# Performance work log

Measured on AMD Instinct MI355X. Metric: run time of the kernel, lower is better.

Reference implementation:

```python
import jax, jax.numpy as jnp
import numpy as np
from jax.scipy.optimize import minimize

LAMDA = 0.01        # lamda default in MI()
N_DOMAINS = 2       # domain_label is binary (source/target)
MAXITER = 50        # BFGS iteration budget (torchmin l-bfgs analogue)


def _sq_dists(A, B):
    # squared euclidean pairwise distances == torch.cdist(A, B, p=2) ** 2
    an = jnp.sum(A * A, axis=-1)
    bn = jnp.sum(B * B, axis=-1)
    return an[:, None] + bn[None, :] - 2.0 * (A @ B.T)


def _median_sigma(sf):
    # sigma = median of nonzero squared pairwise source distances.
    # With continuous features the only zeros are the diagonal, so mask it.
    pd = jnp.maximum(_sq_dists(sf, sf), 0.0)
    pd = jnp.where(jnp.eye(pd.shape[0], dtype=bool), jnp.nan, pd)
    return jnp.nanmedian(pd)


def _build(sf, tf, y, l):
    # Gaussian kernel masked by class agreement, plus domain one-hots.
    sigma = _median_sigma(sf)
    X = jnp.concatenate([sf, tf], axis=0)              # [N, d]
    D = _sq_dists(X, X)                                 # [N, N]
    Deltay = (y[:, None] == y[None, :]).astype(X.dtype)
    K_W = jnp.exp(-D / sigma) * Deltay                  # [N, N]
    onehot = jax.nn.one_hot(l[:, 0], N_DOMAINS, dtype=X.dtype)  # [N, 2]
    KD = K_W * (onehot @ onehot.T)                      # K_W * Deltal
    w = jnp.sum(onehot, axis=0) / X.shape[0]            # domain counts / N
    return K_W, KD, onehot, w


def _div(theta, K_W, KD, onehot, w):
    # mean((K_W*Deltal) @ theta) - mean(exp((theta*K_W) @ Deltal - 1))
    # Deltal = onehot @ onehot.T (rank-2), so the second NxN @ NxN matmul
    # collapses to A = K_W @ (theta[:,None]*onehot) with column weights w.
    term1 = jnp.mean(KD @ theta)
    A = K_W @ (theta[:, None] * onehot)                 # [N, 2]
    term2 = jnp.mean(jnp.exp(A - 1.0) @ w)
    return term1 - term2


def _solve_theta(K_W, KD, onehot, w):
    N = K_W.shape[0]
    obj = lambda th: -_div(th, K_W, KD, onehot, w) + LAMDA * (th @ th)
    res = minimize(obj, jnp.zeros((N,), K_W.dtype), method="BFGS",
                   options={"maxiter": MAXITER})
    return res.x


def setup_inputs() -> dict:
    key = jax.random.key(0)
    k1, k2, k3, k4 = jax.random.split(key, 4)
    B, d, n_class = 2048, 256, 31
    source_features = jax.random.normal(k1, (B, d), dtype=jnp.float32)
    target_features = jax.random.normal(k2, (B, d), dtype=jnp.float32)
    y = jax.random.randint(k3, (2 * B,), 0, n_class, dtype=jnp.int32)
    l = jax.random.randint(k4, (2 * B, 1), 0, N_DOMAINS, dtype=jnp.int32)
    return {"source_features": source_features, "target_features": target_features,
            "y": y, "l": l}


def reference(source_features, target_features, y, l):
    K_W, KD, onehot, w = _build(source_features, target_features, y, l)
    theta_hat = _solve_theta(K_W, KD, onehot, w)
    return _div(theta_hat, K_W, KD, onehot, w)
```

## Files before the change

### kernel.cpp

```cpp
#include <hip/hip_runtime.h>
#include <math.h>

#define N_TOT   4096
#define N_SRC   2048
#define DIMF    256
#define NCLASS  31
#define LAMBDA  0.01f

#define K_TRI1  1048063LL
#define K_TRI2  1048064LL

#define WS_ACC    0
#define WS_HIST0  64
#define WS_HISTA  16448
#define WS_HISTB  32832
#define WS_H2A    49216
#define WS_H2B    50240
#define WS_STATE  51264
#define WS_TICK   51520
#define WS_META   52288
#define WS_SCAL   52800
#define ZERO_BYTES 53248
#define WS_PERM   53248
#define WS_XN     69632
#define WS_DS     1048576
#define WS_KBLK   17825792

#define MAXW 224
#define MAXM 112
#define WPAD 114

__device__ __forceinline__ float bf2f(unsigned short h) {
  return __uint_as_float(((unsigned)h) << 16);
}

__device__ __forceinline__ double blockReduceSum(double v, double* red) {
#pragma unroll
  for (int o = 32; o > 0; o >>= 1) v += __shfl_down(v, o, 64);
  int w = threadIdx.x >> 6, lane = threadIdx.x & 63;
  __syncthreads();
  if (lane == 0) red[w] = v;
  __syncthreads();
  return red[0] + red[1] + red[2] + red[3];
}

__device__ __forceinline__ void blockReduceSumMax(double s, double mx, double* red,
                                                  double& os, double& om) {
#pragma unroll
  for (int o = 32; o > 0; o >>= 1) {
    s += __shfl_down(s, o, 64);
    double u = __shfl_down(mx, o, 64);
    mx = fmax(mx, u);
  }
  int w = threadIdx.x >> 6, lane = threadIdx.x & 63;
  __syncthreads();
  if (lane == 0) { red[w] = s; red[4 + w] = mx; }
  __syncthreads();
  os = red[0] + red[1] + red[2] + red[3];
  om = fmax(fmax(red[4], red[5]), fmax(red[6], red[7]));
}

__device__ void scan_find(const unsigned* hist, int nbins, long long k, unsigned* shOut) {
  __shared__ long long tsum[256];
  int tid = threadIdx.x;
  int per = nbins / 256;
  long long s = 0;
  for (int q = 0; q < per; q++) s += hist[tid * per + q];
  tsum[tid] = s;
  __syncthreads();
  if (tid == 0) {
    long long run = 0;
    for (int t = 0; t < 256; t++) { long long v = tsum[t]; tsum[t] = run; run += v; }
  }
  __syncthreads();
  long long run = tsum[tid];
  for (int q = 0; q < per; q++) {
    unsigned c = hist[tid * per + q];
    if (k >= run && k < run + (long long)c) { shOut[0] = (unsigned)(tid * per + q); shOut[1] = (unsigned)(k - run); }
    run += c;
  }
  __syncthreads();
}

__global__ __launch_bounds__(256) void xn_kernel(const float* __restrict__ sf,
                                                 const float* __restrict__ tf,
                                                 float* __restrict__ xn) {
  int wid = threadIdx.x >> 6, lane = threadIdx.x & 63;
  int row = blockIdx.x * 4 + wid;
  const float* src = (row < N_SRC) ? (sf + (size_t)row * DIMF) : (tf + (size_t)(row - N_SRC) * DIMF);
  float4 v = ((const float4*)src)[lane];
  float s = v.x * v.x + v.y * v.y + v.z * v.z + v.w * v.w;
#pragma unroll
  for (int o = 32; o > 0; o >>= 1) s += __shfl_down(s, o, 64);
  if (lane == 0) xn[row] = s;
}

__global__ __launch_bounds__(256) void dist_k(const float* __restrict__ sf,
                                              const float* __restrict__ xn,
                                              float* __restrict__ Ds,
                                              unsigned* __restrict__ h) {
  __shared__ float As[16][68];
  __shared__ float Bs[16][68];
  __shared__ unsigned lh[4096];
  const int tx = threadIdx.x, ty = threadIdx.y;
  const int tid = ty * 16 + tx;
  for (int q = tid; q < 4096; q += 256) lh[q] = 0;
  int b = blockIdx.x;
  int by = (int)((sqrtf(8.f * (float)b + 1.f) - 1.f) * 0.5f);
  while ((by + 1) * (by + 2) / 2 <= b) ++by;
  while (by * (by + 1) / 2 > b) --by;
  int bx = b - by * (by + 1) / 2;
  const int R = by * 64, C = bx * 64;
  const int si = tid >> 2, sq = tid & 3;
  float4 va = ((const float4*)(sf + (size_t)(R + si) * 256 + 0))[sq];
  float4 vb = ((const float4*)(sf + (size_t)(C + si) * 256 + 0))[sq];
  float acc[4][4] = {};
  for (int kc = 0; kc < 256; kc += 16) {
    As[sq * 4 + 0][si] = va.x; As[sq * 4 + 1][si] = va.y; As[sq * 4 + 2][si] = va.z; As[sq * 4 + 3][si] = va.w;
    Bs[sq * 4 + 0][si] = vb.x; Bs[sq * 4 + 1][si] = vb.y; Bs[sq * 4 + 2][si] = vb.z; Bs[sq * 4 + 3][si] = vb.w;
    __syncthreads();
    if (kc + 16 < 256) {
      va = ((const float4*)(sf + (size_t)(R + si) * 256 + kc + 16))[sq];
      vb = ((const float4*)(sf + (size_t)(C + si) * 256 + kc + 16))[sq];
    }
#pragma unroll
    for (int k = 0; k < 16; k++) {
      float4 a = *(const float4*)&As[k][ty * 4];
      float4 b2 = *(const float4*)&Bs[k][tx * 4];
      acc[0][0] += a.x * b2.x; acc[0][1] += a.x * b2.y; acc[0][2] += a.x * b2.z; acc[0][3] += a.x * b2.w;
      acc[1][0] += a.y * b2.x; acc[1][1] += a.y * b2.y; acc[1][2] += a.y * b2.z; acc[1][3] += a.y * b2.w;
      acc[2][0] += a.z * b2.x; acc[2][1] += a.z * b2.y; acc[2][2] += a.z * b2.z; acc[2][3] += a.z * b2.w;
      acc[3][0] += a.w * b2.x; acc[3][1] += a.w * b2.y; acc[3][2] += a.w * b2.z; acc[3][3] += a.w * b2.w;
    }
    __syncthreads();
  }
  int jbase = C + tx * 4;
  float xnj0 = xn[jbase + 0], xnj1 = xn[jbase + 1], xnj2 = xn[jbase + 2], xnj3 = xn[jbase + 3];
#pragma unroll
  for (int r = 0; r < 4; r++) {
    int i = R + ty * 4 + r;
    float xni = xn[i];
    float v[4];
    v[0] = fmaxf(xni + xnj0 - 2.f * acc[r][0], 0.f);
    v[1] = fmaxf(xni + xnj1 - 2.f * acc[r][1], 0.f);
    v[2] = fmaxf(xni + xnj2 - 2.f * acc[r][2], 0.f);
    v[3] = fmaxf(xni + xnj3 - 2.f * acc[r][3], 0.f);
    if (jbase + 3 < i) {
      float4 o; o.x = v[0]; o.y = v[1]; o.z = v[2]; o.w = v[3];
      ((float4*)&Ds[(size_t)i * 2048 + jbase])[0] = o;
      atomicAdd(&lh[__float_as_uint(v[0]) >> 20], 1u);
      atomicAdd(&lh[__float_as_uint(v[1]) >> 20], 1u);
      atomicAdd(&lh[__float_as_uint(v[2]) >> 20], 1u);
      atomicAdd(&lh[__float_as_uint(v[3]) >> 20], 1u);
    } else {
#pragma unroll
      for (int k = 0; k < 4; k++) {
        if (jbase + k < i) {
          Ds[(size_t)i * 2048 + jbase + k] = v[k];
          atomicAdd(&lh[__float_as_uint(v[k]) >> 20], 1u);
        }
      }
    }
  }
  __syncthreads();
  for (int q = tid; q < 4096; q += 256) if (lh[q]) atomicAdd(&h[q], lh[q]);
}

__global__ __launch_bounds__(256) void scan0_k(const unsigned* __restrict__ h, unsigned* __restrict__ st) {
  __shared__ unsigned r0[2];
  __shared__ unsigned r1[2];
  scan_find(h, 4096, K_TRI1, r0);
  scan_find(h, 4096, K_TRI2, r1);
  if (threadIdx.x == 0) { st[0] = r0[0]; st[1] = r0[1]; st[2] = r1[0]; st[3] = r1[1]; }
}

__global__ __launch_bounds__(256) void hist1_k(const float* __restrict__ Ds, const unsigned* __restrict__ st,
                                               unsigned* __restrict__ hA, unsigned* __restrict__ hB) {
  __shared__ unsigned lA[4096];
  __shared__ unsigned lB[4096];
  for (int i = threadIdx.x; i < 4096; i += 256) { lA[i] = 0; lB[i] = 0; }
  __syncthreads();
  unsigned s0 = st[0], s1 = st[2];
  int gw = (blockIdx.x * 256 + threadIdx.x) >> 6;
  int lane = threadIdx.x & 63;
  const float* row = Ds + (size_t)gw * 2048;
  for (int j = lane; j < gw; j += 64) {
    unsigned u = __float_as_uint(row[j]);
    unsigned hi = u >> 20, mid = (u >> 8) & 0xFFFu;
    if (hi == s0) atomicAdd(&lA[mid], 1u);
    if (hi == s1) atomicAdd(&lB[mid], 1u);
  }
  __syncthreads();
  for (int i = threadIdx.x; i < 4096; i += 256) {
    if (lA[i]) atomicAdd(&hA[i], lA[i]);
    if (lB[i]) atomicAdd(&hB[i], lB[i]);
  }
}

__global__ __launch_bounds__(256) void scan1_k(const unsigned* __restrict__ hA, const unsigned* __restrict__ hB,
                                               unsigned* __restrict__ st) {
  __shared__ unsigned r0[2];
  __shared__ unsigned r1[2];
  long long kA = (long long)st[1];
  long long kB = (long long)st[3];
  scan_find(hA, 4096, kA, r0);
  scan_find(hB, 4096, kB, r1);
  if (threadIdx.x == 0) { st[4] = r0[0]; st[5] = r0[1]; st[6] = r1[0]; st[7] = r1[1]; }
}

__global__ __launch_bounds__(256) void hist2_k(const float* __restrict__ Ds, const unsigned* __restrict__ st,
                                               unsigned* __restrict__ hA, unsigned* __restrict__ hB) {
  __shared__ unsigned lA[256];
  __shared__ unsigned lB[256];
  lA[threadIdx.x] = 0; lB[threadIdx.x] = 0;
  __syncthreads();
  unsigned p0 = (st[0] << 12) | st[4];
  unsigned p1 = (st[2] << 12) | st[6];
  int gw = (blockIdx.x * 256 + threadIdx.x) >> 6;
  int lane = threadIdx.x & 63;
  const float* row = Ds + (size_t)gw * 2048;
  for (int j = lane; j < gw; j += 64) {
    unsigned u = __float_as_uint(row[j]);
    unsigned pre = u >> 8;
    if (pre == p0) atomicAdd(&lA[u & 0xFFu], 1u);
    if (pre == p1) atomicAdd(&lB[u & 0xFFu], 1u);
  }
  __syncthreads();
  if (lA[threadIdx.x]) atomicAdd(&hA[threadIdx.x], lA[threadIdx.x]);
  if (lB[threadIdx.x]) atomicAdd(&hB[threadIdx.x], lB[threadIdx.x]);
}

__global__ __launch_bounds__(256) void scan2b_k(const unsigned* __restrict__ hA, const unsigned* __restrict__ hB,
                                                const unsigned* __restrict__ st, float* __restrict__ scal,
                                                const int* __restrict__ y, const int* __restrict__ l,
                                                int* __restrict__ perm, int* __restrict__ meta) {
  int tid = threadIdx.x;
  __shared__ unsigned r0[2];
  __shared__ unsigned r1[2];
  scan_find(hA, 256, (long long)st[5], r0);
  scan_find(hB, 256, (long long)st[7], r1);
  if (tid == 0) {
    unsigned v1 = (st[0] << 20) | (st[4] << 8) | r0[0];
    unsigned v2 = (st[2] << 20) | (st[6] << 8) | r1[0];
    scal[0] = 0.5f * (__uint_as_float(v1) + __uint_as_float(v2));
  }
  __shared__ unsigned cl[64];
  __shared__ unsigned bs2[64];
  __shared__ unsigned cur[64];
  if (tid < 64) cl[tid] = 0;
  __syncthreads();
  for (int i = tid; i < N_TOT; i += 256) atomicAdd(&cl[y[i] * 2 + l[i]], 1u);
  __syncthreads();
  if (tid == 0) {
    unsigned run = 0;
    for (int b2 = 0; b2 < 62; b2++) { bs2[b2] = run; run += cl[b2]; }
    unsigned run2 = 0, cnt0 = 0;
    for (int c = 0; c < NCLASS; c++) {
      int n = (int)(cl[2 * c] + cl[2 * c + 1]);
      meta[c] = n; meta[32 + c] = (int)cl[2 * c]; meta[64 + c] = (int)bs2[2 * c];
      meta[96 + c] = (int)run2; run2 += (unsigned)(n * n);
      cnt0 += cl[2 * c];
    }
    scal[1] = (float)((double)cnt0 / (4096.0 * 4096.0));
    scal[2] = (float)((double)(N_TOT - cnt0) / (4096.0 * 4096.0));
  }
  __syncthreads();
  if (tid < 64) cur[tid] = bs2[tid];
  __syncthreads();
  for (int i = tid; i < N_TOT; i += 256) {
    int b2 = y[i] * 2 + l[i];
    unsigned pos = atomicAdd(&cur[b2], 1u);
    perm[pos] = i;
  }
}

__global__ __launch_bounds__(256) void build_k(const float* __restrict__ sf, const float* __restrict__ tf,
                                               const float* __restrict__ xn, const int* __restrict__ perm,
                                               const int* __restrict__ meta, const float* __restrict__ scal,
                                               float* __restrict__ gK) {
  const int c = blockIdx.z;
  const int n = meta[c];
  const int cs = meta[64 + c];
  const int bo = meta[96 + c];
  const int T = (n + 15) >> 4;
  int b = blockIdx.x;
  if (b >= T * (T + 1) / 2) return;
  int by = (int)((sqrtf(8.f * (float)b + 1.f) - 1.f) * 0.5f);
  while ((by + 1) * (by + 2) / 2 <= b) ++by;
  while (by * (by + 1) / 2 > b) --by;
  int bx = b - by * (by + 1) / 2;
  const int i0 = by * 16, j0 = bx * 16;
  const int tx = threadIdx.x, ty = threadIdx.y;
  __shared__ float As[16][260];
  __shared__ float Bs[16][260];
  __shared__ float ot[16][17];
  __shared__ int ra[16];
  __shared__ int rb[16];
  int tid = ty * 16 + tx;
  if (tid < 16) { int il = i0 + tid; ra[tid] = (il < n) ? perm[cs + il] : -1; }
  else if (tid < 32) { int jl = j0 + tid - 16; rb[tid - 16] = (jl < n) ? perm[cs + jl] : -1; }
  __syncthreads();
  for (int e = tid; e < 1024; e += 256) {
    int r = e >> 6, q = e & 63;
    int g = ra[r];
    if (g >= 0) {
      const float* src = (g < N_SRC) ? (sf + (size_t)g * DIMF) : (tf + (size_t)(g - N_SRC) * DIMF);
      ((float4*)&As[r][q * 4])[0] = ((const float4*)src)[q];
    }
    int g2 = rb[r];
    if (g2 >= 0) {
      const float* src = (g2 < N_SRC) ? (sf + (size_t)g2 * DIMF) : (tf + (size_t)(g2 - N_SRC) * DIMF);
      ((float4*)&Bs[r][q * 4])[0] = ((const float4*)src)[q];
    }
  }
  __syncthreads();
  int il = i0 + ty, jl = j0 + tx;
  float val = 0.f;
  if (il < n && jl < n) {
    float dot = 0.f;
    const float4* a4 = (const float4*)&As[ty][0];
    const float4* b4 = (const float4*)&Bs[tx][0];
#pragma unroll 16
    for (int q = 0; q < 64; q++) {
      float4 a = a4[q], b2 = b4[q];
      dot += a.x * b2.x + a.y * b2.y + a.z * b2.z + a.w * b2.w;
    }
    int gi = ra[ty], gj = rb[tx];
    float d = xn[gi] + xn[gj] - 2.f * dot;
    val = expf(-d / scal[0]);
    gK[(size_t)bo + (size_t)il * n + jl] = val;
  }
  ot[ty][tx] = val;
  __syncthreads();
  if (by != bx) {
    int il2 = j0 + ty, jl2 = i0 + tx;
    if (il2 < n && jl2 < n) gK[(size_t)bo + (size_t)il2 * n + jl2] = ot[tx][ty];
  }
}

__global__ __launch_bounds__(256) void solver_k(const float* __restrict__ gK, const int* __restrict__ meta,
                                                const float* __restrict__ scal, double* __restrict__ acc,
                                                unsigned* __restrict__ tick, float* __restrict__ out) {
  const int c = blockIdx.x >> 1, d = blockIdx.x & 1;
  const int n = meta[c];
  const int m0 = meta[32 + c];
  const int m = d ? (n - m0) : m0;
  const int c0 = d ? m0 : 0;
  const int bo = meta[96 + c];
  const float gamma = scal[1 + d];
  const int tid = threadIdx.x;
  const int wv = tid >> 6, lane = tid & 63;

  __shared__ unsigned short Wl[MAXW * WPAD];
  __shared__ float pS[4 * MAXM];
  __shared__ float pD[4 * MAXM];
  __shared__ float Av[MAXW];
  __shared__ float Sv[MAXW];
  __shared__ float Uv[MAXW];
  __shared__ float Bq[MAXW];
  __shared__ float bc[MAXM];
  __shared__ float th[MAXM + 1];
  __shared__ float gv[MAXM];
  __shared__ float dgv[MAXM];
  __shared__ float pv[MAXM + 1];
  __shared__ float rv[MAXM + 1];
  __shared__ float zv[MAXM + 1];
  __shared__ float xv[MAXM + 1];
  __shared__ double red[16];

  const float* K = gK + bo;
  const int st = n;
  const int mp2 = (m + 1) & ~1;
  const int iw0 = (n * wv) >> 2, iw1 = (n * (wv + 1)) >> 2;

  for (int i = tid >> 2; i < n; i += 64) {
    const float* Kr = K + (size_t)i * st + c0;
    unsigned short* Wr = Wl + i * WPAD;
    for (int j = (tid & 3); j < m; j += 4) {
      unsigned u = __float_as_uint(Kr[j]);
      u += 0x7fffu + ((u >> 16) & 1u);
      Wr[j] = (unsigned short)(u >> 16);
    }
    if ((tid & 3) == 0 && (m & 1)) Wr[m] = 0;
  }
  {
    const int r0 = (m * wv) >> 2, r1 = (m * (wv + 1)) >> 2;
    for (int j = lane; j < m; j += 64) {
      const float* Kr = K + (size_t)(c0 + j) * st + c0;
      float s = 0.f;
      for (int r = r0; r < r1; r++) s += Kr[r];
      pS[wv * MAXM + j] = s;
    }
  }
  __syncthreads();
  for (int j = tid; j < mp2; j += 256) {
    if (j < m) bc[j] = (pS[j] + pS[MAXM + j] + pS[2 * MAXM + j] + pS[3 * MAXM + j]) * (1.0f / 4096.0f);
    th[j] = 0.f;
  }
  __syncthreads();

  for (int it = 0; it < 25; it++) {
    double o = 0.0;
    if (it == 0) {
      const float s0c = gamma * expf(-1.f);
      for (int i = tid; i < n; i += 256) { Av[i] = 0.f; Sv[i] = s0c; o += (double)s0c; }
    } else {
      for (int i = tid; i < n; i += 256) {
        const unsigned short* Wr = Wl + i * WPAD;
        float a = 0.f;
#pragma unroll 4
        for (int j = 0; j < mp2; j += 2) {
          unsigned u = *(const unsigned*)(Wr + j);
          a += __uint_as_float(u << 16) * th[j]
             + __uint_as_float(u & 0xffff0000u) * th[j + 1];
        }
        Av[i] = a;
        float si = gamma * expf(fminf(a - 1.f, 30.f));
        Sv[i] = si; o += (double)si;
      }
      for (int j = tid; j < m; j += 256) {
        float t_ = th[j];
        o += (double)(-bc[j] * t_ + LAMBDA * t_ * t_);
      }
    }
    __syncthreads();
    if (it == 0) {
      for (int j = lane; j < m; j += 64) {
        const unsigned short* Wc = Wl + j;
        float s_ = 0.f, ds_ = 0.f;
        int i = iw0;
        for (; i + 3 < iw1; i += 4) {
          float w0 = bf2f(Wc[(i + 0) * WPAD]), w1 = bf2f(Wc[(i + 1) * WPAD]);
          float w2 = bf2f(Wc[(i + 2) * WPAD]), w3 = bf2f(Wc[(i + 3) * WPAD]);
          float a0 = w0 * Sv[i], a1 = w1 * Sv[i + 1], a2 = w2 * Sv[i + 2], a3 = w3 * Sv[i + 3];
          s_ += a0 + a1 + a2 + a3;
          ds_ += a0 * w0 + a1 * w1 + a2 * w2 + a3 * w3;
        }
        for (; i < iw1; i++) { float w = bf2f(Wc[i * WPAD]); float a = w * Sv[i]; s_ += a; ds_ += a * w; }
        pS[wv * MAXM + j] = s_; pD[wv * MAXM + j] = ds_;
      }
    } else {
      for (int j = lane; j < m; j += 64) {
        const unsigned short* Wc = Wl + j;
        float s_ = 0.f;
        int i = iw0;
        for (; i + 3 < iw1; i += 4)
          s_ += bf2f(Wc[(i+0)*WPAD]) * Sv[i]   + bf2f(Wc[(i+1)*WPAD]) * Sv[i+1]
              + bf2f(Wc[(i+2)*WPAD]) * Sv[i+2] + bf2f(Wc[(i+3)*WPAD]) * Sv[i+3];
        for (; i < iw1; i++) s_ += bf2f(Wc[i * WPAD]) * Sv[i];
        pS[wv * MAXM + j] = s_;
      }
    }
    __syncthreads();
    double gm = 0.0;
    for (int j = tid; j < m; j += 256) {
      float s_ = pS[j] + pS[MAXM + j] + pS[2 * MAXM + j] + pS[3 * MAXM + j];
      if (it == 0) {
        float ds_ = pD[j] + pD[MAXM + j] + pD[2 * MAXM + j] + pD[3 * MAXM + j];
        dgv[j] = ds_ + 2.f * LAMBDA;
      }
      float g = s_ - bc[j] + 2.f * LAMBDA * th[j];
      gv[j] = g;
      double ag = fabs((double)g); if (ag > gm) gm = ag;
    }
    double obj, gmax;
    blockReduceSumMax(o, gm, red, obj, gmax);
    if (gmax < 1e-5) break;

    const double tolf = (it == 0) ? 1e-2 : ((it == 1) ? 1e-3 : 1e-4);
    double rz = 0.0;
    for (int j = tid; j < mp2; j += 256) {
      float r0 = (j < m) ? -gv[j] : 0.f;
      float z0 = (j < m) ? r0 / dgv[j] : 0.f;
      rv[j] = r0; zv[j] = z0; pv[j] = z0; xv[j] = 0.f;
      rz += (double)r0 * (double)z0;
    }
    rz = blockReduceSum(rz, red);
    double rz0 = rz;
    double gtpacc = 0.0;
    for (int cg = 0; cg < 12; cg++) {
      __syncthreads();
      for (int i = tid; i < n; i += 256) {
        const unsigned short* Wr = Wl + i * WPAD;
        float a = 0.f;
#pragma unroll 4
        for (int j = 0; j < mp2; j += 2) {
          unsigned u = *(const unsigned*)(Wr + j);
          a += __uint_as_float(u << 16) * pv[j]
             + __uint_as_float(u & 0xffff0000u) * pv[j + 1];
        }
        Uv[i] = a * Sv[i];
      }
      __syncthreads();
      for (int j = lane; j < m; j += 64) {
        const unsigned short* Wc = Wl + j;
        float q = 0.f;
        int i = iw0;
        for (; i + 3 < iw1; i += 4)
          q += bf2f(Wc[(i+0)*WPAD]) * Uv[i]   + bf2f(Wc[(i+1)*WPAD]) * Uv[i+1]
             + bf2f(Wc[(i+2)*WPAD]) * Uv[i+2] + bf2f(Wc[(i+3)*WPAD]) * Uv[i+3];
        for (; i < iw1; i++) q += bf2f(Wc[i * WPAD]) * Uv[i];
        pS[wv * MAXM + j] = q;
      }
      __syncthreads();
      double pq = 0.0;
      for (int j = tid; j < m; j += 256) {
        float q = pS[j] + pS[MAXM + j] + pS[2 * MAXM + j] + pS[3 * MAXM + j] + 2.f * LAMBDA * pv[j];
        Bq[j] = q;
        pq += (double)pv[j] * (double)q;
      }
      pq = blockReduceSum(pq, red);
      if (!(pq > 0.0)) break;
      float alpha = (float)(rz / pq);
      gtpacc += (double)alpha * rz;
      double rznew = 0.0;
      for (int j = tid; j < m; j += 256) {
        xv[j] += alpha * pv[j];
        float rn = rv[j] - alpha * Bq[j];
        rv[j] = rn;
        float zn = rn / dgv[j];
        zv[j] = zn;
        rznew += (double)rn * (double)zn;
      }
      rznew = blockReduceSum(rznew, red);
      if (rznew < tolf * rz0 || cg == 11) break;
      float beta = (float)(rznew / rz);
      for (int j = tid; j < m; j += 256) pv[j] = zv[j] + beta * pv[j];
      rz = rznew;
    }
    __syncthreads();
    double gtp = -gtpacc;
    if (!(gtp < 0.0)) break;

    float t = 1.f;
    if (-gtp >= 1e-4) {
      for (int i = tid; i < n; i += 256) {
        const unsigned short* Wr = Wl + i * WPAD;
        float a = 0.f;
#pragma unroll 4
        for (int j = 0; j < mp2; j += 2) {
          unsigned u = *(const unsigned*)(Wr + j);
          a += __uint_as_float(u << 16) * xv[j]
             + __uint_as_float(u & 0xffff0000u) * xv[j + 1];
        }
        Bq[i] = a;
      }
      __syncthreads();
      for (int ls = 0; ls < 10; ls++) {
        double ol = 0.0;
        for (int i = tid; i < n; i += 256)
          ol += (double)(gamma * expf(fminf(Av[i] + t * Bq[i] - 1.f, 30.f)));
        for (int j = tid; j < m; j += 256) {
          float tj = th[j] + t * xv[j];
          ol += (double)(-bc[j] * tj + LAMBDA * tj * tj);
        }
        double ot2 = blockReduceSum(ol, red);
        if (ot2 <= obj + 1e-4 * (double)t * gtp) break;
        t *= 0.5f;
      }
    }
    for (int j = tid; j < mp2; j += 256) th[j] += t * xv[j];
    __syncthreads();
  }

  __syncthreads();
  for (int i = tid; i < n; i += 256) {
    const float* Kr = K + (size_t)i * st + c0;
    float a = 0.f;
    int j = 0;
    for (; j + 7 < m; j += 8)
      a += th[j] * Kr[j] + th[j+1] * Kr[j+1] + th[j+2] * Kr[j+2] + th[j+3] * Kr[j+3]
         + th[j+4] * Kr[j+4] + th[j+5] * Kr[j+5] + th[j+6] * Kr[j+6] + th[j+7] * Kr[j+7];
    for (; j < m; j++) a += th[j] * Kr[j];
    Av[i] = a;
  }
  __syncthreads();
  double t1l = 0.0, t2l = 0.0;
  for (int i = tid; i < n; i += 256) t2l += (double)(gamma * expf(fminf(Av[i] - 1.f, 30.f)));
  for (int j = tid; j < m; j += 256) t1l += (double)(bc[j] * th[j]);
  double t1 = blockReduceSum(t1l, red);
  double t2 = blockReduceSum(t2l, red);
  if (tid == 0) {
    atomicAdd(&acc[0], t1);
    atomicAdd(&acc[1], t2);
    __threadfence();
    unsigned old = __hip_atomic_fetch_add(&tick[0], 1u, __ATOMIC_ACQ_REL, __HIP_MEMORY_SCOPE_AGENT);
    if (old == 61u) {
      double a0 = __hip_atomic_load(&acc[0], __ATOMIC_RELAXED, __HIP_MEMORY_SCOPE_AGENT);
      double a1 = __hip_atomic_load(&acc[1], __ATOMIC_RELAXED, __HIP_MEMORY_SCOPE_AGENT);
      out[0] = (float)(a0 - a1);
    }
  }
}

extern "C" void kernel_launch(void* const* d_in, const int* in_sizes, int n_in,
                              void* d_out, int out_size, void* d_ws, size_t ws_size,
                              hipStream_t stream) {
  const float* sf = (const float*)d_in[0];
  const float* tf = (const float*)d_in[1];
  const int* y = (const int*)d_in[2];
  const int* l = (const int*)d_in[3];
  char* ws = (char*)d_ws;

  double*   acc    = (double*)(ws + WS_ACC);
  unsigned* hist0  = (unsigned*)(ws + WS_HIST0);
  unsigned* histA  = (unsigned*)(ws + WS_HISTA);
  unsigned* histB  = (unsigned*)(ws + WS_HISTB);
  unsigned* h2A    = (unsigned*)(ws + WS_H2A);
  unsigned* h2B    = (unsigned*)(ws + WS_H2B);
  unsigned* state  = (unsigned*)(ws + WS_STATE);
  unsigned* tick   = (unsigned*)(ws + WS_TICK);
  int*      meta   = (int*)(ws + WS_META);
  float*    scal   = (float*)(ws + WS_SCAL);
  int*      perm   = (int*)(ws + WS_PERM);
  float*    xnp    = (float*)(ws + WS_XN);
  float*    Ds     = (float*)(ws + WS_DS);
  float*    gK     = (float*)(ws + WS_KBLK);

  hipMemsetAsync(d_ws, 0, ZERO_BYTES, stream);
  hipLaunchKernelGGL(xn_kernel, dim3(1024), dim3(256), 0, stream, sf, tf, xnp);
  hipLaunchKernelGGL(dist_k, dim3(528), dim3(16, 16), 0, stream, sf, xnp, Ds, hist0);
  hipLaunchKernelGGL(scan0_k, dim3(1), dim3(256), 0, stream, hist0, state);
  hipLaunchKernelGGL(hist1_k, dim3(512), dim3(256), 0, stream, Ds, state, histA, histB);
  hipLaunchKernelGGL(scan1_k, dim3(1), dim3(256), 0, stream, histA, histB, state);
  hipLaunchKernelGGL(hist2_k, dim3(512), dim3(256), 0, stream, Ds, state, h2A, h2B);
  hipLaunchKernelGGL(scan2b_k, dim3(1), dim3(256), 0, stream, h2A, h2B, state, scal, y, l, perm, meta);
  hipLaunchKernelGGL(build_k, dim3(105, 1, NCLASS), dim3(16, 16), 0, stream, sf, tf, xnp, perm, meta, scal, gK);
  hipLaunchKernelGGL(solver_k, dim3(62), dim3(256), 0, stream, gK, meta, scal, acc, tick, (float*)d_out);
}
```

Baseline: 230.4 us.

## Run CG vector updates in one wavefront, widen matvec loads, parallelize scan

The conjugate-gradient scalar and vector updates now run in registers of a single wavefront, using shuffle-based float reductions. This replaces several block-wide double reductions and their __syncthreads per CG step with one shared stop flag. The row matvecs read four bf16 weights and a float4 of the vector per step, which needs the row pad widened to 116 and the vector arrays padded to 128. The serial single-thread prefix scan in the histogram search becomes a log-step parallel scan. In exchange, CG reductions drop from double to float precision and the other three wavefronts sit idle during the vector updates.

```diff
diff --git a/kernel.cpp b/kernel.cpp
--- a/kernel.cpp
+++ b/kernel.cpp
@@ -28,10 +28,16 @@
 
 #define MAXW 224
 #define MAXM 112
-#define WPAD 114
+#define WPAD 116
 
 __device__ __forceinline__ float bf2f(unsigned short h) {
   return __uint_as_float(((unsigned)h) << 16);
+}
+
+__device__ __forceinline__ float wredF(float v) {
+#pragma unroll
+  for (int o = 1; o < 64; o <<= 1) v += __shfl_xor(v, o, 64);
+  return v;
 }
 
 __device__ __forceinline__ double blockReduceSum(double v, double* red) {
@@ -68,12 +74,15 @@
   for (int q = 0; q < per; q++) s += hist[tid * per + q];
   tsum[tid] = s;
   __syncthreads();
-  if (tid == 0) {
-    long long run = 0;
-    for (int t = 0; t < 256; t++) { long long v = tsum[t]; tsum[t] = run; run += v; }
-  }
-  __syncthreads();
-  long long run = tsum[tid];
+  long long acc = s;
+  for (int off = 1; off < 256; off <<= 1) {
+    long long add = (tid >= off) ? tsum[tid - off] : 0;
+    __syncthreads();
+    acc += add;
+    tsum[tid] = acc;
+    __syncthreads();
+  }
+  long long run = acc - s;
   for (int q = 0; q < per; q++) {
     unsigned c = hist[tid * per + q];
     if (k >= run && k < run + (long long)c) { shOut[0] = (unsigned)(tid * per + q); shOut[1] = (unsigned)(k - run); }
@@ -359,18 +368,19 @@
   __shared__ float Uv[MAXW];
   __shared__ float Bq[MAXW];
   __shared__ float bc[MAXM];
-  __shared__ float th[MAXM + 1];
   __shared__ float gv[MAXM];
   __shared__ float dgv[MAXM];
-  __shared__ float pv[MAXM + 1];
-  __shared__ float rv[MAXM + 1];
-  __shared__ float zv[MAXM + 1];
-  __shared__ float xv[MAXM + 1];
+  __shared__ alignas(16) float th[128];
+  __shared__ alignas(16) float pv[128];
+  __shared__ alignas(16) float xv[128];
   __shared__ double red[16];
+  __shared__ double gds[2];
+  __shared__ int cgst[2];
 
   const float* K = gK + bo;
   const int st = n;
   const int mp2 = (m + 1) & ~1;
+  const int mp4 = (m + 3) & ~3;
   const int iw0 = (n * wv) >> 2, iw1 = (n * (wv + 1)) >> 2;
 
   for (int i = tid >> 2; i < n; i += 64) {
@@ -381,7 +391,7 @@
       u += 0x7fffu + ((u >> 16) & 1u);
       Wr[j] = (unsigned short)(u >> 16);
     }
-    if ((tid & 3) == 0 && (m & 1)) Wr[m] = 0;
+    if ((tid & 3) == 0) for (int j = m; j < mp4; j++) Wr[j] = 0;
   }
   {
     const int r0 = (m * wv) >> 2, r1 = (m * (wv + 1)) >> 2;
@@ -393,10 +403,9 @@
     }
   }
   __syncthreads();
-  for (int j = tid; j < mp2; j += 256) {
-    if (j < m) bc[j] = (pS[j] + pS[MAXM + j] + pS[2 * MAXM + j] + pS[3 * MAXM + j]) * (1.0f / 4096.0f);
-    th[j] = 0.f;
-  }
+  for (int j = tid; j < 128; j += 256) { th[j] = 0.f; pv[j] = 0.f; xv[j] = 0.f; }
+  for (int j = tid; j < m; j += 256)
+    bc[j] = (pS[j] + pS[MAXM + j] + pS[2 * MAXM + j] + pS[3 * MAXM + j]) * (1.0f / 4096.0f);
   __syncthreads();
 
   for (int it = 0; it < 25; it++) {
@@ -409,10 +418,14 @@
         const unsigned short* Wr = Wl + i * WPAD;
         float a = 0.f;
 #pragma unroll 4
-        for (int j = 0; j < mp2; j += 2) {
-          unsigned u = *(const unsigned*)(Wr + j);
-          a += __uint_as_float(u << 16) * th[j]
-             + __uint_as_float(u & 0xffff0000u) * th[j + 1];
+        for (int j = 0; j < mp4; j += 4) {
+          unsigned long long u = *(const unsigned long long*)(Wr + j);
+          float4 t4 = *(const float4*)(th + j);
+          unsigned lo = (unsigned)u, hi = (unsigned)(u >> 32);
+          a += __uint_as_float(lo << 16) * t4.x
+             + __uint_as_float(lo & 0xffff0000u) * t4.y
+             + __uint_as_float(hi << 16) * t4.z
+             + __uint_as_float(hi & 0xffff0000u) * t4.w;
         }
         Av[i] = a;
         float si = gamma * expf(fminf(a - 1.f, 30.f));
@@ -467,27 +480,35 @@
     blockReduceSumMax(o, gm, red, obj, gmax);
     if (gmax < 1e-5) break;
 
-    const double tolf = (it == 0) ? 1e-2 : ((it == 1) ? 1e-3 : 1e-4);
-    double rz = 0.0;
-    for (int j = tid; j < mp2; j += 256) {
-      float r0 = (j < m) ? -gv[j] : 0.f;
-      float z0 = (j < m) ? r0 / dgv[j] : 0.f;
-      rv[j] = r0; zv[j] = z0; pv[j] = z0; xv[j] = 0.f;
-      rz += (double)r0 * (double)z0;
-    }
-    rz = blockReduceSum(rz, red);
-    double rz0 = rz;
+    const float tolf = (it == 0) ? 1e-2f : ((it == 1) ? 1e-3f : 1e-4f);
+    float p0 = 0.f, p1 = 0.f, r0 = 0.f, r1 = 0.f, z0 = 0.f, z1 = 0.f, x0 = 0.f, x1 = 0.f;
+    float dg0 = 1.f, dg1 = 1.f, rzf = 0.f, rz0f = 0.f;
     double gtpacc = 0.0;
+    const int j0 = lane, j1 = lane + 64;
+    if (wv == 0) {
+      if (j0 < m) { dg0 = dgv[j0]; r0 = -gv[j0]; z0 = r0 / dg0; }
+      if (j1 < m) { dg1 = dgv[j1]; r1 = -gv[j1]; z1 = r1 / dg1; }
+      p0 = z0; p1 = z1;
+      rzf = wredF(r0 * z0 + r1 * z1);
+      rz0f = rzf;
+      pv[j0] = p0; pv[j1] = p1;
+      if (lane == 0) cgst[0] = (rzf > 0.f) ? 0 : 1;
+    }
+    __syncthreads();
     for (int cg = 0; cg < 12; cg++) {
-      __syncthreads();
+      if (cgst[0]) break;
       for (int i = tid; i < n; i += 256) {
         const unsigned short* Wr = Wl + i * WPAD;
         float a = 0.f;
 #pragma unroll 4
-        for (int j = 0; j < mp2; j += 2) {
-          unsigned u = *(const unsigned*)(Wr + j);
-          a += __uint_as_float(u << 16) * pv[j]
-             + __uint_as_float(u & 0xffff0000u) * pv[j + 1];
+        for (int j = 0; j < mp4; j += 4) {
+          unsigned long long u = *(const unsigned long long*)(Wr + j);
+          float4 t4 = *(const float4*)(pv + j);
+          unsigned lo = (unsigned)u, hi = (unsigned)(u >> 32);
+          a += __uint_as_float(lo << 16) * t4.x
+             + __uint_as_float(lo & 0xffff0000u) * t4.y
+             + __uint_as_float(hi << 16) * t4.z
+             + __uint_as_float(hi & 0xffff0000u) * t4.w;
         }
         Uv[i] = a * Sv[i];
       }
@@ -503,33 +524,38 @@
         pS[wv * MAXM + j] = q;
       }
       __syncthreads();
-      double pq = 0.0;
-      for (int j = tid; j < m; j += 256) {
-        float q = pS[j] + pS[MAXM + j] + pS[2 * MAXM + j] + pS[3 * MAXM + j] + 2.f * LAMBDA * pv[j];
-        Bq[j] = q;
-        pq += (double)pv[j] * (double)q;
-      }
-      pq = blockReduceSum(pq, red);
-      if (!(pq > 0.0)) break;
-      float alpha = (float)(rz / pq);
-      gtpacc += (double)alpha * rz;
-      double rznew = 0.0;
-      for (int j = tid; j < m; j += 256) {
-        xv[j] += alpha * pv[j];
-        float rn = rv[j] - alpha * Bq[j];
-        rv[j] = rn;
-        float zn = rn / dgv[j];
-        zv[j] = zn;
-        rznew += (double)rn * (double)zn;
-      }
-      rznew = blockReduceSum(rznew, red);
-      if (rznew < tolf * rz0 || cg == 11) break;
-      float beta = (float)(rznew / rz);
-      for (int j = tid; j < m; j += 256) pv[j] = zv[j] + beta * pv[j];
-      rz = rznew;
-    }
-    __syncthreads();
-    double gtp = -gtpacc;
+      if (wv == 0) {
+        float q0 = 0.f, q1 = 0.f;
+        if (j0 < m) q0 = pS[j0] + pS[MAXM + j0] + pS[2*MAXM + j0] + pS[3*MAXM + j0] + 2.f * LAMBDA * p0;
+        if (j1 < m) q1 = pS[j1] + pS[MAXM + j1] + pS[2*MAXM + j1] + pS[3*MAXM + j1] + 2.f * LAMBDA * p1;
+        float pq = wredF(p0 * q0 + p1 * q1);
+        int stop = 0;
+        if (!(pq > 0.f)) stop = 1;
+        else {
+          float alpha = rzf / pq;
+          gtpacc += (double)alpha * (double)rzf;
+          x0 += alpha * p0; x1 += alpha * p1;
+          r0 -= alpha * q0; r1 -= alpha * q1;
+          z0 = r0 / dg0;    z1 = r1 / dg1;
+          float rzn = wredF(r0 * z0 + r1 * z1);
+          if (rzn < tolf * rz0f || cg == 11) stop = 1;
+          else {
+            float beta = rzn / rzf;
+            p0 = z0 + beta * p0; p1 = z1 + beta * p1;
+            pv[j0] = p0; pv[j1] = p1;
+            rzf = rzn;
+          }
+        }
+        if (lane == 0) cgst[0] = stop;
+      }
+      __syncthreads();
+    }
+    if (wv == 0) {
+      xv[j0] = x0; xv[j1] = x1;
+      if (lane == 0) gds[0] = -gtpacc;
+    }
+    __syncthreads();
+    double gtp = gds[0];
     if (!(gtp < 0.0)) break;
 
     float t = 1.f;
@@ -538,10 +564,14 @@
         const unsigned short* Wr = Wl + i * WPAD;
         float a = 0.f;
 #pragma unroll 4
-        for (int j = 0; j < mp2; j += 2) {
-          unsigned u = *(const unsigned*)(Wr + j);
-          a += __uint_as_float(u << 16) * xv[j]
-             + __uint_as_float(u & 0xffff0000u) * xv[j + 1];
+        for (int j = 0; j < mp4; j += 4) {
+          unsigned long long u = *(const unsigned long long*)(Wr + j);
+          float4 t4 = *(const float4*)(xv + j);
+          unsigned lo = (unsigned)u, hi = (unsigned)(u >> 32);
+          a += __uint_as_float(lo << 16) * t4.x
+             + __uint_as_float(lo & 0xffff0000u) * t4.y
+             + __uint_as_float(hi << 16) * t4.z
+             + __uint_as_float(hi & 0xffff0000u) * t4.w;
         }
         Bq[i] = a;
       }
```

New measurement: 209.3 us. 1.1x faster.
